# Optimization experiments

Hardware: AMD Instinct MI355X
Metric: run time of the kernel (lower is better)

Reference implementation:

```python
import jax, jax.numpy as jnp
import numpy as np

D_MODEL = 1024
D_STATE = 16
D_CONV = 4
EXPAND = 2
D_INNER = EXPAND * D_MODEL
DT_RANK = (D_MODEL + 15) // 16  # ceil(d_model/16) = 64
BATCH, SEQ = 4, 4096


def setup_inputs() -> dict:
    key = jax.random.key(0)
    ks = jax.random.split(key, 8)
    s = 0.02
    x = jax.random.normal(ks[0], (BATCH, SEQ, D_MODEL), jnp.float32)
    in_proj_w = jax.random.normal(ks[1], (2 * D_INNER, D_MODEL), jnp.float32) * s
    conv_w = jax.random.normal(ks[2], (D_INNER, D_CONV), jnp.float32) * 0.2  # depthwise kernel
    conv_b = jnp.zeros((D_INNER,), jnp.float32)
    x_proj_w = jax.random.normal(ks[3], (DT_RANK + 2 * D_STATE, D_INNER), jnp.float32) * s
    dt_proj_w = jax.random.normal(ks[4], (D_INNER, DT_RANK), jnp.float32) * s
    # standard mamba dt bias init: softplus(bias) ~ small positive dt
    dt_proj_b = jnp.log(jnp.expm1(jnp.full((D_INNER,), 1e-2, jnp.float32)))
    # S4D-real init: A = -[1..d_state] per channel
    A_log = jnp.log(jnp.tile(jnp.arange(1, D_STATE + 1, dtype=jnp.float32), (D_INNER, 1)))
    D_skip = jnp.ones((D_INNER,), jnp.float32)
    out_proj_w = jax.random.normal(ks[5], (D_MODEL, D_INNER), jnp.float32) * s
    return dict(x=x, in_proj_w=in_proj_w, conv_w=conv_w, conv_b=conv_b,
                x_proj_w=x_proj_w, dt_proj_w=dt_proj_w, dt_proj_b=dt_proj_b,
                A_log=A_log, D_skip=D_skip, out_proj_w=out_proj_w)


def _rmsnorm(x, eps=1e-6):
    # FastSimpleRMSNorm: no learned weight
    return x * jax.lax.rsqrt(jnp.mean(x * x, axis=-1, keepdims=True) + eps)


def reference(x, in_proj_w, conv_w, conv_b, x_proj_w, dt_proj_w, dt_proj_b,
              A_log, D_skip, out_proj_w):
    B_, L, _ = x.shape
    u = _rmsnorm(x)
    # in_proj -> gate z and conv branch xc, each [B, L, d_inner]
    xz = jnp.einsum('bld,ed->ble', u, in_proj_w)
    xc, z = jnp.split(xz, 2, axis=-1)
    # causal depthwise conv1d (width D_CONV) + silu
    xp = jnp.pad(xc, ((0, 0), (D_CONV - 1, 0), (0, 0)))
    conv = conv_b + sum(conv_w[:, k] * xp[:, k:k + L, :] for k in range(D_CONV))
    xc = jax.nn.silu(conv)
    # x_proj -> dt, B, C
    dbl = jnp.einsum('ble,fe->blf', xc, x_proj_w)
    dt, Bm, Cm = jnp.split(dbl, [DT_RANK, DT_RANK + D_STATE], axis=-1)
    dt = jax.nn.softplus(jnp.einsum('blr,er->ble', dt, dt_proj_w) + dt_proj_b)  # [B,L,d_inner]
    A = -jnp.exp(A_log)  # [d_inner, d_state]

    def step(h, inp):
        dt_t, B_t, C_t, x_t = inp  # [B,d_inner],[B,d_state],[B,d_state],[B,d_inner]
        dA = jnp.exp(dt_t[..., None] * A)             # [B,d_inner,d_state]
        h = h * dA + (dt_t * x_t)[..., None] * B_t[:, None, :]
        y = jnp.einsum('bes,bs->be', h, C_t)
        return h, y

    h0 = jnp.zeros((B_, D_INNER, D_STATE), xc.dtype)
    xs = (jnp.swapaxes(dt, 0, 1), jnp.swapaxes(Bm, 0, 1),
          jnp.swapaxes(Cm, 0, 1), jnp.swapaxes(xc, 0, 1))
    _, ys = jax.lax.scan(step, h0, xs)                # [L,B,d_inner]
    y = jnp.swapaxes(ys, 0, 1) + D_skip * xc
    y = y * jax.nn.silu(z)
    out = jnp.einsum('ble,de->bld', y, out_proj_w)
    return x + out
```

## Files before the change

kernel.cpp:

```cpp
#include <hip/hip_runtime.h>
#include <hip/hip_bf16.h>
#include <math.h>

typedef __hip_bfloat16 bf16;
typedef __attribute__((ext_vector_type(8))) short short8;
typedef __attribute__((ext_vector_type(4))) float f32x4;

#define BATCH_N 4
#define SEQ_N 4096
#define DMODEL 1024
#define DINNER 2048
#define DTRANK 64
#define DSTATE 16
#define NROWS (BATCH_N * SEQ_N)

__device__ __forceinline__ float b2f(bf16 v) { return __bfloat162float(v); }
__device__ __forceinline__ bf16 f2b(float v) { return __float2bfloat16(v); }

__device__ __forceinline__ void gll16(const bf16* g, bf16* l) {
    __builtin_amdgcn_global_load_lds((const __attribute__((address_space(1))) unsigned int*)g,
                                     (__attribute__((address_space(3))) unsigned int*)l,
                                     16, 0, 0);
}

#define CVT_N1 4194304
#define CVT_N2 196608
#define CVT_N3 131072
#define CVT_N4 2097152
__global__ void cvt_all_kernel(const float* __restrict__ i1, bf16* __restrict__ o1,
                               const float* __restrict__ i2, bf16* __restrict__ o2,
                               const float* __restrict__ i3, bf16* __restrict__ o3,
                               const float* __restrict__ i4, bf16* __restrict__ o4) {
    int i = blockIdx.x * 256 + threadIdx.x;
    if (i < CVT_N1) { o1[i] = f2b(i1[i]); }
    i -= CVT_N1;
    if (i >= 0 && i < CVT_N2) { o2[i] = f2b(i2[i]); }
    i -= CVT_N2;
    if (i >= 0 && i < CVT_N3) { o3[i] = f2b(i3[i]); }
    i -= CVT_N3;
    if (i >= 0 && i < CVT_N4) { o4[i] = f2b(i4[i]); }
}

__global__ __launch_bounds__(256) void rmsnorm_kernel(const float* __restrict__ x, bf16* __restrict__ u) {
    const int r = blockIdx.x;
    const int t = threadIdx.x;
    const float4 v = reinterpret_cast<const float4*>(x + (size_t)r * DMODEL)[t];
    float ss = v.x * v.x + v.y * v.y + v.z * v.z + v.w * v.w;
    #pragma unroll
    for (int o = 32; o > 0; o >>= 1) ss += __shfl_down(ss, o);
    __shared__ float red[4];
    if ((t & 63) == 0) red[t >> 6] = ss;
    __syncthreads();
    const float tot = red[0] + red[1] + red[2] + red[3];
    const float rs = rsqrtf(tot * (1.0f / DMODEL) + 1e-6f);
    union { uint2 u2; bf16 h[4]; } o4;
    o4.h[0] = f2b(v.x * rs); o4.h[1] = f2b(v.y * rs);
    o4.h[2] = f2b(v.z * rs); o4.h[3] = f2b(v.w * rs);
    *reinterpret_cast<uint2*>(u + (size_t)r * DMODEL + t * 4) = o4.u2;
}

__global__ __launch_bounds__(256) void conv_silu_kernel(const bf16* __restrict__ xcraw,
                                                        const float* __restrict__ cw,
                                                        const float* __restrict__ cb,
                                                        bf16* __restrict__ xc) {
    const int idx = blockIdx.x * 256 + threadIdx.x;
    const int e = idx & (DINNER - 1);
    const int r = idx >> 11;
    const int l = r & (SEQ_N - 1);
    const float4 w = *reinterpret_cast<const float4*>(cw + e * 4);
    float xs[4];
    #pragma unroll
    for (int k = 0; k < 4; ++k) {
        const int lp = l - 3 + k;
        xs[k] = (lp >= 0) ? b2f(xcraw[(size_t)(r - 3 + k) * DINNER + e]) : 0.f;
    }
    const float acc = cb[e] + w.x * xs[0] + w.y * xs[1] + w.z * xs[2] + w.w * xs[3];
    xc[idx] = f2b(acc / (1.f + __expf(-acc)));
}

template <int EPI>
__global__ __launch_bounds__(256) void mfma_gemm(const bf16* __restrict__ A,
                                                 const bf16* __restrict__ B,
                                                 void* __restrict__ Cout,
                                                 void* __restrict__ Cout2,
                                                 const float* __restrict__ aux,
                                                 int N, int K) {
    __shared__ __align__(16) bf16 sA[128 * 32];
    __shared__ __align__(16) bf16 sB[128 * 32];
    const int tid = threadIdx.x;
    const int w = tid >> 6;
    const int lane = tid & 63;
    const int quad = lane >> 4;
    const int l15 = lane & 15;
    const int m0 = blockIdx.x * 128;
    const int n0 = blockIdx.y * 128;
    const int wm = (w >> 1) * 64;
    const int wn = (w & 1) * 64;

    f32x4 acc[4][4];
    #pragma unroll
    for (int i = 0; i < 4; ++i)
        #pragma unroll
        for (int j = 0; j < 4; ++j)
            acc[i][j] = (f32x4){0.f, 0.f, 0.f, 0.f};

    const int sm = tid >> 2;
    const int q = (tid & 3) ^ ((sm >> 1) & 3);
    const bf16* gA0 = A + (size_t)(m0 + sm) * K + q * 8;
    const bf16* gA1 = gA0 + (size_t)64 * K;
    const bf16* gB0 = B + (size_t)(n0 + sm) * K + q * 8;
    const bf16* gB1 = gB0 + (size_t)64 * K;
    bf16* lA0 = sA + w * 512;
    bf16* lA1 = sA + 2048 + w * 512;
    bf16* lB0 = sB + w * 512;
    bf16* lB1 = sB + 2048 + w * 512;

    const int sw2 = (l15 >> 1) & 3;
    const int qx = (quad ^ sw2) * 8;

    for (int k0 = 0; k0 < K; k0 += 32) {
        gll16(gA0 + k0, lA0);
        gll16(gA1 + k0, lA1);
        gll16(gB0 + k0, lB0);
        gll16(gB1 + k0, lB1);
        __syncthreads();
        short8 af[4], bfr[4];
        #pragma unroll
        for (int f = 0; f < 4; ++f) {
            af[f]  = *reinterpret_cast<const short8*>(sA + (wm + f * 16 + l15) * 32 + qx);
            bfr[f] = *reinterpret_cast<const short8*>(sB + (wn + f * 16 + l15) * 32 + qx);
        }
        #pragma unroll
        for (int i = 0; i < 4; ++i)
            #pragma unroll
            for (int j = 0; j < 4; ++j)
                acc[i][j] = __builtin_amdgcn_mfma_f32_16x16x32_bf16(af[i], bfr[j], acc[i][j], 0, 0, 0);
        __syncthreads();
    }

    const int rbase = m0 + wm + quad * 4;
    if constexpr (EPI == 1) {
        bf16* C = (bf16*)Cout;
        #pragma unroll
        for (int i = 0; i < 4; ++i)
            #pragma unroll
            for (int r = 0; r < 4; ++r) {
                const size_t ro = (size_t)(rbase + i * 16 + r) * N;
                #pragma unroll
                for (int j = 0; j < 4; ++j) {
                    const int c = n0 + wn + j * 16 + l15;
                    float v = acc[i][j][r] + aux[c];
                    if (v < 15.f) v = __logf(1.f + __expf(v));
                    C[ro + c] = f2b(v);
                }
            }
    } else if constexpr (EPI == 2) {
        float* C = (float*)Cout;
        #pragma unroll
        for (int i = 0; i < 4; ++i)
            #pragma unroll
            for (int r = 0; r < 4; ++r) {
                const size_t ro = (size_t)(rbase + i * 16 + r) * N;
                #pragma unroll
                for (int j = 0; j < 4; ++j) {
                    const int c = n0 + wn + j * 16 + l15;
                    C[ro + c] = acc[i][j][r] + aux[ro + c];
                }
            }
    } else if constexpr (EPI == 3) {
        bf16* C = (bf16*)((n0 < 2048) ? Cout : Cout2);
        const int cb = (n0 & 2047) + wn;
        #pragma unroll
        for (int i = 0; i < 4; ++i)
            #pragma unroll
            for (int r = 0; r < 4; ++r) {
                const size_t ro = (size_t)(rbase + i * 16 + r) * 2048;
                #pragma unroll
                for (int j = 0; j < 4; ++j)
                    C[ro + cb + j * 16 + l15] = f2b(acc[i][j][r]);
            }
    } else {
        bf16* Cd = (bf16*)Cout;
        float* Cbc = (float*)Cout2;
        #pragma unroll
        for (int i = 0; i < 4; ++i)
            #pragma unroll
            for (int r = 0; r < 4; ++r) {
                const size_t row = (size_t)(rbase + i * 16 + r);
                #pragma unroll
                for (int j = 0; j < 4; ++j) {
                    const int c = wn + j * 16 + l15;
                    if (c < 64) Cd[row * 64 + c] = f2b(acc[i][j][r]);
                    else if (c < 96) Cbc[row * 32 + (c - 64)] = acc[i][j][r];
                }
            }
    }
}

__device__ __forceinline__ bool pow_ok(const float* a) {
    bool ok = true;
    #pragma unroll
    for (int s = 1; s < 16; ++s) {
        const float t = a[0] * (s + 1);
        ok = ok && (fabsf(a[s] - t) <= 1e-4f * fabsf(t) + 1e-6f);
    }
    return ok;
}

template <int NC>
__global__ __launch_bounds__(256) void scan_passA(const bf16* __restrict__ dt,
                                                  const bf16* __restrict__ xc,
                                                  const float* __restrict__ bcbuf,
                                                  const float* __restrict__ A_log,
                                                  float* __restrict__ hend,
                                                  float* __restrict__ sumdt) {
    constexpr int LC = SEQ_N / NC;
    const int e = blockIdx.x * 256 + threadIdx.x;
    const int c = blockIdx.y;
    const int b = blockIdx.z;
    float a[16], h[16];
    #pragma unroll
    for (int s = 0; s < 16; ++s) {
        a[s] = -__expf(A_log[e * 16 + s]);
        h[s] = 0.f;
    }
    const bool pw = pow_ok(a);
    float sd = 0.f;
    const size_t rbase = (size_t)b * SEQ_N + (size_t)c * LC;
    for (int i = 0; i < LC; ++i) {
        const size_t row = rbase + i;
        const float dtv = b2f(dt[row * DINNER + e]);
        const float xv = b2f(xc[row * DINNER + e]);
        const float cdx = dtv * xv;
        const float4* bp = reinterpret_cast<const float4*>(bcbuf + row * 32);
        float Bv[16];
        *reinterpret_cast<float4*>(&Bv[0])  = bp[0];
        *reinterpret_cast<float4*>(&Bv[4])  = bp[1];
        *reinterpret_cast<float4*>(&Bv[8])  = bp[2];
        *reinterpret_cast<float4*>(&Bv[12]) = bp[3];
        sd += dtv;
        if (pw) {
            const float e1 = __expf(dtv * a[0]);
            float dAp = 1.f;
            #pragma unroll
            for (int s = 0; s < 16; ++s) {
                dAp *= e1;
                h[s] = fmaf(h[s], dAp, cdx * Bv[s]);
            }
        } else {
            #pragma unroll
            for (int s = 0; s < 16; ++s) {
                const float dA = __expf(dtv * a[s]);
                h[s] = fmaf(h[s], dA, cdx * Bv[s]);
            }
        }
    }
    const size_t o = ((size_t)b * NC + c) * DINNER + e;
    #pragma unroll
    for (int s = 0; s < 16; s += 4) {
        float4 v = {h[s], h[s + 1], h[s + 2], h[s + 3]};
        *reinterpret_cast<float4*>(hend + o * 16 + s) = v;
    }
    sumdt[o] = sd;
}

template <int NC>
__global__ __launch_bounds__(256) void scan_passB(float* hstate,
                                                  const float* __restrict__ sumdt,
                                                  const float* __restrict__ A_log) {
    const int g = blockIdx.x * 256 + threadIdx.x;
    const int s = g & 15;
    const int e = (g >> 4) & (DINNER - 1);
    const int b = g >> 15;
    const float a = -__expf(A_log[e * 16 + s]);
    float H = 0.f;
    for (int c = 0; c < NC; ++c) {
        const size_t o = ((size_t)b * NC + c) * DINNER + e;
        const float he = hstate[o * 16 + s];
        const float sd = sumdt[o];
        hstate[o * 16 + s] = H;
        H = fmaf(H, __expf(a * sd), he);
    }
}

template <int NC>
__global__ __launch_bounds__(256) void scan_passC(const bf16* dt,
                                                  const bf16* __restrict__ xc,
                                                  const bf16* __restrict__ z,
                                                  const float* __restrict__ bcbuf,
                                                  const float* __restrict__ A_log,
                                                  const float* __restrict__ D_skip,
                                                  const float* __restrict__ hinit,
                                                  bf16* y) {
    constexpr int LC = SEQ_N / NC;
    const int e = blockIdx.x * 256 + threadIdx.x;
    const int c = blockIdx.y;
    const int b = blockIdx.z;
    float a[16], h[16];
    #pragma unroll
    for (int s = 0; s < 16; ++s) a[s] = -__expf(A_log[e * 16 + s]);
    const bool pw = pow_ok(a);
    const float dsk = D_skip[e];
    const size_t o = ((size_t)b * NC + c) * DINNER + e;
    #pragma unroll
    for (int s = 0; s < 16; s += 4) {
        float4 v = *reinterpret_cast<const float4*>(hinit + o * 16 + s);
        h[s] = v.x; h[s + 1] = v.y; h[s + 2] = v.z; h[s + 3] = v.w;
    }
    const size_t rbase = (size_t)b * SEQ_N + (size_t)c * LC;
    for (int i = 0; i < LC; ++i) {
        const size_t row = rbase + i;
        const float dtv = b2f(dt[row * DINNER + e]);
        const float xv = b2f(xc[row * DINNER + e]);
        const float zv = b2f(z[row * DINNER + e]);
        const float cdx = dtv * xv;
        const float4* bp = reinterpret_cast<const float4*>(bcbuf + row * 32);
        float Bv[16], Cv[16];
        *reinterpret_cast<float4*>(&Bv[0])  = bp[0];
        *reinterpret_cast<float4*>(&Bv[4])  = bp[1];
        *reinterpret_cast<float4*>(&Bv[8])  = bp[2];
        *reinterpret_cast<float4*>(&Bv[12]) = bp[3];
        *reinterpret_cast<float4*>(&Cv[0])  = bp[4];
        *reinterpret_cast<float4*>(&Cv[4])  = bp[5];
        *reinterpret_cast<float4*>(&Cv[8])  = bp[6];
        *reinterpret_cast<float4*>(&Cv[12]) = bp[7];
        float yv = 0.f;
        if (pw) {
            const float e1 = __expf(dtv * a[0]);
            float dAp = 1.f;
            #pragma unroll
            for (int s = 0; s < 16; ++s) {
                dAp *= e1;
                h[s] = fmaf(h[s], dAp, cdx * Bv[s]);
                yv = fmaf(h[s], Cv[s], yv);
            }
        } else {
            #pragma unroll
            for (int s = 0; s < 16; ++s) {
                const float dA = __expf(dtv * a[s]);
                h[s] = fmaf(h[s], dA, cdx * Bv[s]);
                yv = fmaf(h[s], Cv[s], yv);
            }
        }
        const float g = (yv + dsk * xv) * (zv / (1.f + __expf(-zv)));
        y[row * DINNER + e] = f2b(g);
    }
}

extern "C" void kernel_launch(void* const* d_in, const int* in_sizes, int n_in,
                              void* d_out, int out_size, void* d_ws, size_t ws_size,
                              hipStream_t stream) {
    const float* x         = (const float*)d_in[0];
    const float* in_proj_w = (const float*)d_in[1];
    const float* conv_w    = (const float*)d_in[2];
    const float* conv_b    = (const float*)d_in[3];
    const float* x_proj_w  = (const float*)d_in[4];
    const float* dt_proj_w = (const float*)d_in[5];
    const float* dt_proj_b = (const float*)d_in[6];
    const float* A_log     = (const float*)d_in[7];
    const float* D_skip    = (const float*)d_in[8];
    const float* out_proj_w= (const float*)d_in[9];
    float* out = (float*)d_out;

    char* ws = (char*)d_ws;
    bf16*  xcraw = (bf16*)(ws + 0);
    bf16*  xc    = (bf16*)(ws + 67108864);
    bf16*  dtr   = (bf16*)(ws + 134217728);
    float* bcbuf = (float*)(ws + 136314880);
    bf16*  w_in  = (bf16*)(ws + 140509184);
    bf16*  w_xp  = (bf16*)(ws + 148897792);
    bf16*  w_dt  = (bf16*)(ws + 149422080);
    bf16*  w_out = (bf16*)(ws + 149684224);
    float* hend  = (float*)(ws + 153878528);
    bf16*  u     = xc;
    bf16*  dtb   = xcraw;
    bf16*  yb    = dtb;
    bf16*  zbuf  = (bf16*)d_out;

    const bool big = (ws_size >= 189530112ULL);
    float* sumdt = (float*)(ws + (big ? 187432960 : 170655744));

    {
        const int total = CVT_N1 + CVT_N2 + CVT_N3 + CVT_N4;
        cvt_all_kernel<<<(total + 255) / 256, 256, 0, stream>>>(
            in_proj_w, w_in, x_proj_w, w_xp, dt_proj_w, w_dt, out_proj_w, w_out);
    }

    rmsnorm_kernel<<<NROWS, 256, 0, stream>>>(x, u);
    mfma_gemm<3><<<dim3(NROWS / 128, 4096 / 128), 256, 0, stream>>>(
        u, w_in, xcraw, zbuf, nullptr, 4096, DMODEL);
    conv_silu_kernel<<<(NROWS * DINNER) / 256, 256, 0, stream>>>(xcraw, conv_w, conv_b, xc);
    mfma_gemm<4><<<dim3(NROWS / 128, 1), 256, 0, stream>>>(
        xc, w_xp, dtr, bcbuf, nullptr, 128, DINNER);
    mfma_gemm<1><<<dim3(NROWS / 128, DINNER / 128), 256, 0, stream>>>(
        dtr, w_dt, dtb, nullptr, dt_proj_b, DINNER, DTRANK);
    if (big) {
        scan_passA<64><<<dim3(DINNER / 256, 64, BATCH_N), 256, 0, stream>>>(
            dtb, xc, bcbuf, A_log, hend, sumdt);
        scan_passB<64><<<(BATCH_N * DINNER * DSTATE) / 256, 256, 0, stream>>>(hend, sumdt, A_log);
        scan_passC<64><<<dim3(DINNER / 256, 64, BATCH_N), 256, 0, stream>>>(
            dtb, xc, zbuf, bcbuf, A_log, D_skip, hend, yb);
    } else {
        scan_passA<32><<<dim3(DINNER / 256, 32, BATCH_N), 256, 0, stream>>>(
            dtb, xc, bcbuf, A_log, hend, sumdt);
        scan_passB<32><<<(BATCH_N * DINNER * DSTATE) / 256, 256, 0, stream>>>(hend, sumdt, A_log);
        scan_passC<32><<<dim3(DINNER / 256, 32, BATCH_N), 256, 0, stream>>>(
            dtb, xc, zbuf, bcbuf, A_log, D_skip, hend, yb);
    }
    mfma_gemm<2><<<dim3(NROWS / 128, DMODEL / 128), 256, 0, stream>>>(
        yb, w_out, out, nullptr, x, DMODEL, DINNER);
    (void)in_sizes; (void)n_in; (void)out_size;
}
```

Baseline: 770.2 us.

## Split-K the x_proj GEMM, double K-step GEMM loop, vectorize conv

The x_proj GEMM ran only 128 blocks, so it now uses split-K over two halves writing fp32 partials that a new combine kernel sums and scatters into dt and B/C buffers. The shared GEMM loop now loads two 32-wide K chunks per barrier pair, halving synchronizations at the cost of doubling LDS use per block. The conv+silu kernel handles four channels per thread with vector loads and stores. The combine pass adds an extra launch and fp32 partial traffic, and the partial buffers reuse the hend workspace.

```diff
diff --git a/kernel.cpp b/kernel.cpp
--- a/kernel.cpp
+++ b/kernel.cpp
@@ -59,34 +59,53 @@
     *reinterpret_cast<uint2*>(u + (size_t)r * DMODEL + t * 4) = o4.u2;
 }
 
-__global__ __launch_bounds__(256) void conv_silu_kernel(const bf16* __restrict__ xcraw,
-                                                        const float* __restrict__ cw,
-                                                        const float* __restrict__ cb,
-                                                        bf16* __restrict__ xc) {
-    const int idx = blockIdx.x * 256 + threadIdx.x;
-    const int e = idx & (DINNER - 1);
-    const int r = idx >> 11;
+__global__ __launch_bounds__(256) void conv_silu4_kernel(const bf16* __restrict__ xcraw,
+                                                         const float* __restrict__ cw,
+                                                         const float* __restrict__ cb,
+                                                         bf16* __restrict__ xc) {
+    const int t = blockIdx.x * 256 + threadIdx.x;
+    const int e = (t << 2) & (DINNER - 1);
+    const int r = t >> 9;
     const int l = r & (SEQ_N - 1);
-    const float4 w = *reinterpret_cast<const float4*>(cw + e * 4);
-    float xs[4];
+    float4 w0 = *reinterpret_cast<const float4*>(cw + (e + 0) * 4);
+    float4 w1 = *reinterpret_cast<const float4*>(cw + (e + 1) * 4);
+    float4 w2 = *reinterpret_cast<const float4*>(cw + (e + 2) * 4);
+    float4 w3 = *reinterpret_cast<const float4*>(cw + (e + 3) * 4);
+    const float4 bias = *reinterpret_cast<const float4*>(cb + e);
+    float xs[4][4];
     #pragma unroll
     for (int k = 0; k < 4; ++k) {
         const int lp = l - 3 + k;
-        xs[k] = (lp >= 0) ? b2f(xcraw[(size_t)(r - 3 + k) * DINNER + e]) : 0.f;
-    }
-    const float acc = cb[e] + w.x * xs[0] + w.y * xs[1] + w.z * xs[2] + w.w * xs[3];
-    xc[idx] = f2b(acc / (1.f + __expf(-acc)));
+        if (lp >= 0) {
+            union { uint2 u; bf16 h[4]; } tmp;
+            tmp.u = *reinterpret_cast<const uint2*>(xcraw + (size_t)(r - 3 + k) * DINNER + e);
+            #pragma unroll
+            for (int j = 0; j < 4; ++j) xs[k][j] = b2f(tmp.h[j]);
+        } else {
+            #pragma unroll
+            for (int j = 0; j < 4; ++j) xs[k][j] = 0.f;
+        }
+    }
+    float acc[4];
+    acc[0] = bias.x + w0.x * xs[0][0] + w0.y * xs[1][0] + w0.z * xs[2][0] + w0.w * xs[3][0];
+    acc[1] = bias.y + w1.x * xs[0][1] + w1.y * xs[1][1] + w1.z * xs[2][1] + w1.w * xs[3][1];
+    acc[2] = bias.z + w2.x * xs[0][2] + w2.y * xs[1][2] + w2.z * xs[2][2] + w2.w * xs[3][2];
+    acc[3] = bias.w + w3.x * xs[0][3] + w3.y * xs[1][3] + w3.z * xs[2][3] + w3.w * xs[3][3];
+    union { uint2 u; bf16 h[4]; } o;
+    #pragma unroll
+    for (int j = 0; j < 4; ++j) o.h[j] = f2b(acc[j] / (1.f + __expf(-acc[j])));
+    *reinterpret_cast<uint2*>(xc + (size_t)r * DINNER + e) = o.u;
 }
 
 template <int EPI>
-__global__ __launch_bounds__(256) void mfma_gemm(const bf16* __restrict__ A,
-                                                 const bf16* __restrict__ B,
+__global__ __launch_bounds__(256) void mfma_gemm(const bf16* __restrict__ A, int lda,
+                                                 const bf16* __restrict__ B, int ldb,
                                                  void* __restrict__ Cout,
                                                  void* __restrict__ Cout2,
                                                  const float* __restrict__ aux,
                                                  int N, int K) {
-    __shared__ __align__(16) bf16 sA[128 * 32];
-    __shared__ __align__(16) bf16 sB[128 * 32];
+    __shared__ __align__(16) bf16 sA[2][128 * 32];
+    __shared__ __align__(16) bf16 sB[2][128 * 32];
     const int tid = threadIdx.x;
     const int w = tid >> 6;
     const int lane = tid & 63;
@@ -97,6 +116,12 @@
     const int wm = (w >> 1) * 64;
     const int wn = (w & 1) * 64;
 
+    if constexpr (EPI == 5) {
+        const int koff = blockIdx.z * K;
+        A += koff;
+        B += koff;
+    }
+
     f32x4 acc[4][4];
     #pragma unroll
     for (int i = 0; i < 4; ++i)
@@ -106,35 +131,46 @@
 
     const int sm = tid >> 2;
     const int q = (tid & 3) ^ ((sm >> 1) & 3);
-    const bf16* gA0 = A + (size_t)(m0 + sm) * K + q * 8;
-    const bf16* gA1 = gA0 + (size_t)64 * K;
-    const bf16* gB0 = B + (size_t)(n0 + sm) * K + q * 8;
-    const bf16* gB1 = gB0 + (size_t)64 * K;
-    bf16* lA0 = sA + w * 512;
-    bf16* lA1 = sA + 2048 + w * 512;
-    bf16* lB0 = sB + w * 512;
-    bf16* lB1 = sB + 2048 + w * 512;
+    const bf16* gA0 = A + (size_t)(m0 + sm) * lda + q * 8;
+    const bf16* gA1 = gA0 + (size_t)64 * lda;
+    const bf16* gB0 = B + (size_t)(n0 + sm) * ldb + q * 8;
+    const bf16* gB1 = gB0 + (size_t)64 * ldb;
+    bf16* lA0c0 = sA[0] + w * 512;
+    bf16* lA1c0 = sA[0] + 2048 + w * 512;
+    bf16* lA0c1 = sA[1] + w * 512;
+    bf16* lA1c1 = sA[1] + 2048 + w * 512;
+    bf16* lB0c0 = sB[0] + w * 512;
+    bf16* lB1c0 = sB[0] + 2048 + w * 512;
+    bf16* lB0c1 = sB[1] + w * 512;
+    bf16* lB1c1 = sB[1] + 2048 + w * 512;
 
     const int sw2 = (l15 >> 1) & 3;
     const int qx = (quad ^ sw2) * 8;
 
-    for (int k0 = 0; k0 < K; k0 += 32) {
-        gll16(gA0 + k0, lA0);
-        gll16(gA1 + k0, lA1);
-        gll16(gB0 + k0, lB0);
-        gll16(gB1 + k0, lB1);
+    for (int k0 = 0; k0 < K; k0 += 64) {
+        gll16(gA0 + k0, lA0c0);
+        gll16(gA1 + k0, lA1c0);
+        gll16(gB0 + k0, lB0c0);
+        gll16(gB1 + k0, lB1c0);
+        gll16(gA0 + k0 + 32, lA0c1);
+        gll16(gA1 + k0 + 32, lA1c1);
+        gll16(gB0 + k0 + 32, lB0c1);
+        gll16(gB1 + k0 + 32, lB1c1);
         __syncthreads();
-        short8 af[4], bfr[4];
-        #pragma unroll
-        for (int f = 0; f < 4; ++f) {
-            af[f]  = *reinterpret_cast<const short8*>(sA + (wm + f * 16 + l15) * 32 + qx);
-            bfr[f] = *reinterpret_cast<const short8*>(sB + (wn + f * 16 + l15) * 32 + qx);
+        #pragma unroll
+        for (int ch = 0; ch < 2; ++ch) {
+            short8 af[4], bfr[4];
+            #pragma unroll
+            for (int f = 0; f < 4; ++f) {
+                af[f]  = *reinterpret_cast<const short8*>(sA[ch] + (wm + f * 16 + l15) * 32 + qx);
+                bfr[f] = *reinterpret_cast<const short8*>(sB[ch] + (wn + f * 16 + l15) * 32 + qx);
+            }
+            #pragma unroll
+            for (int i = 0; i < 4; ++i)
+                #pragma unroll
+                for (int j = 0; j < 4; ++j)
+                    acc[i][j] = __builtin_amdgcn_mfma_f32_16x16x32_bf16(af[i], bfr[j], acc[i][j], 0, 0, 0);
         }
-        #pragma unroll
-        for (int i = 0; i < 4; ++i)
-            #pragma unroll
-            for (int j = 0; j < 4; ++j)
-                acc[i][j] = __builtin_amdgcn_mfma_f32_16x16x32_bf16(af[i], bfr[j], acc[i][j], 0, 0, 0);
         __syncthreads();
     }
 
@@ -180,21 +216,29 @@
                     C[ro + cb + j * 16 + l15] = f2b(acc[i][j][r]);
             }
     } else {
-        bf16* Cd = (bf16*)Cout;
-        float* Cbc = (float*)Cout2;
+        float* C = (float*)Cout + (size_t)blockIdx.z * NROWS * N;
         #pragma unroll
         for (int i = 0; i < 4; ++i)
             #pragma unroll
             for (int r = 0; r < 4; ++r) {
-                const size_t row = (size_t)(rbase + i * 16 + r);
+                const size_t ro = (size_t)(rbase + i * 16 + r) * N;
                 #pragma unroll
-                for (int j = 0; j < 4; ++j) {
-                    const int c = wn + j * 16 + l15;
-                    if (c < 64) Cd[row * 64 + c] = f2b(acc[i][j][r]);
-                    else if (c < 96) Cbc[row * 32 + (c - 64)] = acc[i][j][r];
-                }
-            }
-    }
+                for (int j = 0; j < 4; ++j)
+                    C[ro + n0 + wn + j * 16 + l15] = acc[i][j][r];
+            }
+    }
+}
+
+__global__ __launch_bounds__(256) void combine_xproj(const float* __restrict__ p0,
+                                                     const float* __restrict__ p1,
+                                                     bf16* __restrict__ dtr,
+                                                     float* __restrict__ bcbuf) {
+    const int idx = blockIdx.x * 256 + threadIdx.x;
+    const int c = idx & 127;
+    const int row = idx >> 7;
+    const float v = p0[idx] + p1[idx];
+    if (c < 64) dtr[(size_t)row * 64 + c] = f2b(v);
+    else if (c < 96) bcbuf[(size_t)row * 32 + (c - 64)] = v;
 }
 
 __device__ __forceinline__ bool pow_ok(const float* a) {
@@ -376,6 +420,8 @@
     bf16*  dtb   = xcraw;
     bf16*  yb    = dtb;
     bf16*  zbuf  = (bf16*)d_out;
+    float* xp_p0 = hend;
+    float* xp_p1 = hend + (size_t)NROWS * 128;
 
     const bool big = (ws_size >= 189530112ULL);
     float* sumdt = (float*)(ws + (big ? 187432960 : 170655744));
@@ -388,12 +434,13 @@
 
     rmsnorm_kernel<<<NROWS, 256, 0, stream>>>(x, u);
     mfma_gemm<3><<<dim3(NROWS / 128, 4096 / 128), 256, 0, stream>>>(
-        u, w_in, xcraw, zbuf, nullptr, 4096, DMODEL);
-    conv_silu_kernel<<<(NROWS * DINNER) / 256, 256, 0, stream>>>(xcraw, conv_w, conv_b, xc);
-    mfma_gemm<4><<<dim3(NROWS / 128, 1), 256, 0, stream>>>(
-        xc, w_xp, dtr, bcbuf, nullptr, 128, DINNER);
+        u, DMODEL, w_in, DMODEL, xcraw, zbuf, nullptr, 4096, DMODEL);
+    conv_silu4_kernel<<<(NROWS * DINNER) / 1024, 256, 0, stream>>>(xcraw, conv_w, conv_b, xc);
+    mfma_gemm<5><<<dim3(NROWS / 128, 1, 2), 256, 0, stream>>>(
+        xc, DINNER, w_xp, DINNER, xp_p0, nullptr, nullptr, 128, DINNER / 2);
+    combine_xproj<<<(NROWS * 128) / 256, 256, 0, stream>>>(xp_p0, xp_p1, dtr, bcbuf);
     mfma_gemm<1><<<dim3(NROWS / 128, DINNER / 128), 256, 0, stream>>>(
-        dtr, w_dt, dtb, nullptr, dt_proj_b, DINNER, DTRANK);
+        dtr, DTRANK, w_dt, DTRANK, dtb, nullptr, dt_proj_b, DINNER, DTRANK);
     if (big) {
         scan_passA<64><<<dim3(DINNER / 256, 64, BATCH_N), 256, 0, stream>>>(
             dtb, xc, bcbuf, A_log, hend, sumdt);
@@ -408,6 +455,6 @@
             dtb, xc, zbuf, bcbuf, A_log, D_skip, hend, yb);
     }
     mfma_gemm<2><<<dim3(NROWS / 128, DMODEL / 128), 256, 0, stream>>>(
-        yb, w_out, out, nullptr, x, DMODEL, DINNER);
+        yb, DINNER, w_out, DINNER, out, nullptr, x, DMODEL, DINNER);
     (void)in_sizes; (void)n_in; (void)out_size;
 }
```

Measured after the change: 712.6 us. -7.5%, faster.
